# Optimization experiments

Hardware: AMD Instinct MI355X
Metric: run time of the kernel (lower is better)

The kernel has to match this reference:

```python
import jax, jax.numpy as jnp
import numpy as np

N, E, C, H, W = 5000, 80000, 32, 8, 8


def setup_inputs() -> dict:
    key = jax.random.key(0)
    k1, k2, k3, k4, k5, k6 = jax.random.split(key, 6)
    h = jax.random.normal(k1, (N, C, H, W), dtype=jnp.float32)
    e = jax.random.uniform(k2, (E,), dtype=jnp.float32)
    src = jax.random.randint(k3, (E,), 0, N, dtype=jnp.int32)
    # ensure every node receives at least one message (avoids -inf segments),
    # matching a connected graph where update_all covers all nodes
    dst = jnp.concatenate([jnp.arange(N, dtype=jnp.int32),
                           jax.random.randint(k4, (E - N,), 0, N, dtype=jnp.int32)])
    fan_in = C * 3 * 3
    bound = float(1.0 / np.sqrt(fan_in))
    conv_w = jax.random.uniform(k5, (C, C, 3, 3), minval=-bound, maxval=bound, dtype=jnp.float32)
    conv_b = jax.random.uniform(k6, (C,), minval=-bound, maxval=bound, dtype=jnp.float32)
    return {"h": h, "e": e, "conv_w": conv_w, "conv_b": conv_b, "src": src, "dst": dst}


def reference(h, e, conv_w, conv_b, src, dst):
    # message: gather source features per edge, scale by scalar edge weight
    m = e[:, None, None, None] * h[src]                      # [E, C, H, W]
    # conv2d(dim->dim, k=3, pad=1) + exact GELU, edges as batch dim
    m = jax.lax.conv_general_dilated(
        m, conv_w, window_strides=(1, 1), padding='SAME',
        dimension_numbers=('NCHW', 'OIHW', 'NCHW'))
    m = jax.nn.gelu(m + conv_b[None, :, None, None], approximate=False)
    # reduce: ragged max over each destination node's mailbox
    out = jax.ops.segment_max(m, dst, num_segments=h.shape[0])  # [N, C, H, W]
    return out
```

## Files before the change

kernel.cpp:

```cpp
#include <hip/hip_runtime.h>
#include <math.h>

#define CCH   32
#define HWPIX 64
#define CHW   2048
#define HT_STRIDE 40
#define HT_NODE   2600

typedef __attribute__((ext_vector_type(8))) short bf16x8;
typedef __attribute__((ext_vector_type(4))) float f32x4;
typedef unsigned int uint_t;
typedef unsigned short ushort_t;

__device__ __forceinline__ ushort_t f2bf(float f) {
    uint_t u = __float_as_uint(f);
    u += 0x7fffu + ((u >> 16) & 1u);
    return (ushort_t)(u >> 16);
}

__device__ __forceinline__ float fgelu(float x) {
    float x2 = x * x;
    float t = x * fmaf(0.0713548162726f, x2, 1.5957691216f);
    float ez = __expf(-t);
    return x * __builtin_amdgcn_rcpf(1.0f + ez);
}


__global__ __launch_bounds__(256) void hist_prep_kernel(
    const int* __restrict__ dst, int* cnt, int ne, int nhist,
    const float* __restrict__ w, ushort_t* __restrict__ wfrag) {
    int b = blockIdx.x;
    if (b < nhist) {
        int i = b * 256 + threadIdx.x;
        if (i < ne) atomicAdd(&cnt[dst[i]], 1);
    } else {
        for (int idx = threadIdx.x; idx < 18 * 64; idx += 256) {
            int ch = idx / (9 * 64);
            int rem = idx % (9 * 64);
            int tap = rem / 64;
            int l = rem % 64;
            int co = ch * 16 + (l & 15);
            int g = l >> 4;
            for (int j = 0; j < 8; j++) {
                int ci = g * 8 + j;
                wfrag[(size_t)idx * 8 + j] = f2bf(w[(co * CCH + ci) * 9 + tap]);
            }
        }
    }
}

__global__ __launch_bounds__(256) void scan_kernel(const int* __restrict__ cnt,
                                                   int* __restrict__ offs,
                                                   int* __restrict__ cursor,
                                                   int nn) {
    __shared__ int part[256];
    int t = threadIdx.x;
    int per = (nn + 255) >> 8;
    if (per > 32) per = 32;
    int base = t * per;
    int local[32];
    int sum = 0;
    for (int i = 0; i < per; i++) {
        int idx = base + i;
        int v = (idx < nn) ? cnt[idx] : 0;
        local[i] = sum;
        sum += v;
    }
    part[t] = sum;
    __syncthreads();
    int acc = sum;
    for (int d = 1; d < 256; d <<= 1) {
        int tv = (t >= d) ? part[t - d] : 0;
        __syncthreads();
        acc += tv;
        part[t] = acc;
        __syncthreads();
    }
    int excl = acc - sum;
    for (int i = 0; i < per; i++) {
        int idx = base + i;
        if (idx < nn) {
            int o = excl + local[i];
            offs[idx] = o;
            cursor[idx] = o;
        }
    }
    if (t == 255) offs[nn] = acc;
}

__global__ __launch_bounds__(256) void conv_scatter_kernel(
    const float* __restrict__ h, const ushort_t* __restrict__ wfrag,
    ushort_t* __restrict__ convh, int nconv,
    const int* __restrict__ dst, const int* __restrict__ src,
    const float* __restrict__ e, int* cursor, int2* __restrict__ swA, int ne) {
    __shared__ ushort_t Ht[2 * HT_NODE];
    int b = blockIdx.x;
    int t = threadIdx.x;

    if (b >= nconv) {
        int i = (b - nconv) * 256 + t;
        if (i < ne) {
            int p = atomicAdd(&cursor[dst[i]], 1);
            int2 v;
            v.x = src[i];
            v.y = __float_as_int(e[i]);
            swA[p] = v;
        }
        return;
    }

    int node0 = b * 2;
    uint_t* Hd = (uint_t*)Ht;
#pragma unroll
    for (int nd = 0; nd < 2; nd++) {
        const float* hn = h + (size_t)(node0 + nd) * CHW;
#pragma unroll
        for (int it = 0; it < 4; it++) {
            int ci2 = it * 4 + (t >> 6);
            int p = t & 63;
            float a = hn[ci2 * 128 + p];
            float bb = hn[ci2 * 128 + 64 + p];
            uint_t val = (uint_t)f2bf(a) | ((uint_t)f2bf(bb) << 16);
            Hd[nd * (HT_NODE / 2) + p * (HT_STRIDE / 2) + ci2] = val;
        }
    }
    if (t < 40) Hd[0 * (HT_NODE / 2) + 64 * (HT_STRIDE / 2) + (t % 20)] = 0;
    if (t >= 40 && t < 80) Hd[1 * (HT_NODE / 2) + 64 * (HT_STRIDE / 2) + (t - 40) % 20] = 0;
    __syncthreads();

    int l = t & 63;
    int w = __builtin_amdgcn_readfirstlane(t >> 6);
    int nd = w >> 1;
    int ch = w & 1;
    int s = l & 15, g = l >> 4;
    int n = node0 + nd;

    bf16x8 A[9];
#pragma unroll
    for (int tap = 0; tap < 9; tap++)
        A[tap] = ((const bf16x8*)wfrag)[(ch * 9 + tap) * 64 + l];

    f32x4 C[4];
#pragma unroll
    for (int i = 0; i < 4; i++) C[i] = (f32x4){0.f, 0.f, 0.f, 0.f};

    const short* HtS = (const short*)(Ht + nd * HT_NODE);
#pragma unroll
    for (int tau = 0; tau < 4; tau++) {
        int p = tau * 16 + s;
        int y = p >> 3, x = p & 7;
#pragma unroll
        for (int tap = 0; tap < 9; tap++) {
            int dy = tap / 3 - 1, dx = tap % 3 - 1;
            int yy = y + dy, xx = x + dx;
            bool valid = (yy >= 0) & (yy < 8) & (xx >= 0) & (xx < 8);
            int pp = valid ? (yy * 8 + xx) : 64;
            bf16x8 B = *(const bf16x8*)&HtS[pp * HT_STRIDE + g * 8];
            C[tau] = __builtin_amdgcn_mfma_f32_16x16x32_bf16(A[tap], B, C[tau], 0, 0, 0);
        }
    }

    ushort_t* outn = convh + (size_t)n * CHW;
#pragma unroll
    for (int tau = 0; tau < 4; tau++) {
        uint_t lo = (uint_t)f2bf(C[tau][0]) | ((uint_t)f2bf(C[tau][1]) << 16);
        uint_t hi = (uint_t)f2bf(C[tau][2]) | ((uint_t)f2bf(C[tau][3]) << 16);
        uint2 v; v.x = lo; v.y = hi;
        *(uint2*)(outn + (tau * 16 + s) * 32 + ch * 16 + g * 4) = v;
    }
}

__device__ __forceinline__ void red8(float* mn, float* mx, uint4 q, float wg) {
    uint_t u0 = q.x, u1 = q.y, u2 = q.z, u3 = q.w;
    float v;
    v = wg * __uint_as_float(u0 << 16);          mn[0] = fminf(mn[0], v); mx[0] = fmaxf(mx[0], v);
    v = wg * __uint_as_float(u0 & 0xffff0000u);  mn[1] = fminf(mn[1], v); mx[1] = fmaxf(mx[1], v);
    v = wg * __uint_as_float(u1 << 16);          mn[2] = fminf(mn[2], v); mx[2] = fmaxf(mx[2], v);
    v = wg * __uint_as_float(u1 & 0xffff0000u);  mn[3] = fminf(mn[3], v); mx[3] = fmaxf(mx[3], v);
    v = wg * __uint_as_float(u2 << 16);          mn[4] = fminf(mn[4], v); mx[4] = fmaxf(mx[4], v);
    v = wg * __uint_as_float(u2 & 0xffff0000u);  mn[5] = fminf(mn[5], v); mx[5] = fmaxf(mx[5], v);
    v = wg * __uint_as_float(u3 << 16);          mn[6] = fminf(mn[6], v); mx[6] = fmaxf(mx[6], v);
    v = wg * __uint_as_float(u3 & 0xffff0000u);  mn[7] = fminf(mn[7], v); mx[7] = fmaxf(mx[7], v);
}

__global__ __launch_bounds__(256) void gather_max_kernel(
    const ushort_t* __restrict__ convh, const float* __restrict__ bias,
    const int* __restrict__ offs, const int2* __restrict__ swA,
    float* __restrict__ out) {
    int t = threadIdx.x;
    int l = t & 63;
    int w = t >> 6;
    int b = blockIdx.x;
    int q = b & 3;
    int n = (b >> 2) * 4 + w;
    int beg = offs[n], end = offs[n + 1];
    int last = end - 1;

    const char* qbase = (const char*)convh + 1024 * q + 16 * l;

    float mn[8], mx[8];
#pragma unroll
    for (int i = 0; i < 8; i++) { mn[i] = 3.402823466e+38f; mx[i] = -3.402823466e+38f; }

    int j1 = (beg + 1 < last) ? beg + 1 : last;
    int j2 = (beg + 2 < last) ? beg + 2 : last;
    int j3 = (beg + 3 < last) ? beg + 3 : last;
    int2 d0 = swA[beg], d1 = swA[j1], d2 = swA[j2], d3 = swA[j3];
    uint4 Q0 = *(const uint4*)(qbase + (size_t)d0.x * 4096);
    uint4 Q1 = *(const uint4*)(qbase + (size_t)d1.x * 4096);
    uint4 Q2 = *(const uint4*)(qbase + (size_t)d2.x * 4096);
    uint4 Q3 = *(const uint4*)(qbase + (size_t)d3.x * 4096);
    float W0 = __int_as_float(d0.y), W1 = __int_as_float(d1.y);
    float W2 = __int_as_float(d2.y), W3 = __int_as_float(d3.y);
    int k0 = (beg + 4 < last) ? beg + 4 : last;
    int k1 = (beg + 5 < last) ? beg + 5 : last;
    int k2 = (beg + 6 < last) ? beg + 6 : last;
    int k3 = (beg + 7 < last) ? beg + 7 : last;
    int2 S0 = swA[k0], S1 = swA[k1], S2 = swA[k2], S3 = swA[k3];

    for (int j = beg; j < end; j += 4) {
        int m0 = (j + 8 < last) ? j + 8 : last;
        int m1 = (j + 9 < last) ? j + 9 : last;
        int m2 = (j + 10 < last) ? j + 10 : last;
        int m3 = (j + 11 < last) ? j + 11 : last;
        int2 N0 = swA[m0], N1 = swA[m1], N2 = swA[m2], N3 = swA[m3];
        red8(mn, mx, Q0, W0);
        Q0 = *(const uint4*)(qbase + (size_t)S0.x * 4096); W0 = __int_as_float(S0.y);
        red8(mn, mx, Q1, W1);
        Q1 = *(const uint4*)(qbase + (size_t)S1.x * 4096); W1 = __int_as_float(S1.y);
        red8(mn, mx, Q2, W2);
        Q2 = *(const uint4*)(qbase + (size_t)S2.x * 4096); W2 = __int_as_float(S2.y);
        red8(mn, mx, Q3, W3);
        Q3 = *(const uint4*)(qbase + (size_t)S3.x * 4096); W3 = __int_as_float(S3.y);
        S0 = N0; S1 = N1; S2 = N2; S3 = N3;
    }

    const float4* b4 = (const float4*)(bias + (l & 3) * 8);
    float4 bLo = b4[0], bHi = b4[1];
    float bb[8] = {bLo.x, bLo.y, bLo.z, bLo.w, bHi.x, bHi.y, bHi.z, bHi.w};
    float* op = out + (size_t)n * CHW + (size_t)(l & 3) * 512 + q * 16 + (l >> 2);
#pragma unroll
    for (int i = 0; i < 8; i++) {
        op[i * 64] = fmaxf(fgelu(mx[i] + bb[i]), fgelu(mn[i] + bb[i]));
    }
}

extern "C" void kernel_launch(void* const* d_in, const int* in_sizes, int n_in,
                              void* d_out, int out_size, void* d_ws, size_t ws_size,
                              hipStream_t stream) {
    const float* h      = (const float*)d_in[0];
    const float* e      = (const float*)d_in[1];
    const float* conv_w = (const float*)d_in[2];
    const float* conv_b = (const float*)d_in[3];
    const int*   src    = (const int*)d_in[4];
    const int*   dst    = (const int*)d_in[5];
    int nn = in_sizes[0] / CHW;
    int ne = in_sizes[1];

    ushort_t* convh = (ushort_t*)d_ws;
    ushort_t* wfrag = convh + (size_t)nn * CHW;
    int*   cnt    = (int*)(wfrag + 18 * 64 * 8);
    int*   offs   = cnt + nn;
    int*   cursor = offs + nn + 2;
    int2*  swA    = (int2*)(cursor + nn);

    int nhist = (ne + 255) / 256;
    int nconv = nn / 2;

    hipMemsetAsync(cnt, 0, (size_t)nn * sizeof(int), stream);
    hist_prep_kernel<<<nhist + 1, 256, 0, stream>>>(dst, cnt, ne, nhist,
                                                    conv_w, wfrag);
    scan_kernel<<<1, 256, 0, stream>>>(cnt, offs, cursor, nn);
    conv_scatter_kernel<<<nconv + nhist, 256, 0, stream>>>(
        h, wfrag, convh, nconv, dst, src, e, cursor, swA, ne);
    gather_max_kernel<<<nn, 256, 0, stream>>>(convh, conv_b, offs, swA,
                                              (float*)d_out);
}
```

Baseline: 153.7 us.

## Fuse scan into histogram via last-block pattern and split gather across half-waves

The histogram/weight-prep kernel now ends with an atomic completion counter, and the last block to finish performs the prefix scan, removing a separate single-block scan launch. The gather-max kernel is split into twice as many blocks, each covering half the per-node slice. Within a wave the two 32-lane halves process alternating edges and are combined with a cross-half shuffle before the GELU and store. This is meant to cut launch overhead and raise parallelism and memory-level concurrency in the gather. In exchange it adds atomics and a relaxed-load dependency in the scan, and uses half the lanes during the epilogue.

```diff
diff --git a/kernel.cpp b/kernel.cpp
--- a/kernel.cpp
+++ b/kernel.cpp
@@ -25,16 +25,17 @@
     return x * __builtin_amdgcn_rcpf(1.0f + ez);
 }
 
-
-__global__ __launch_bounds__(256) void hist_prep_kernel(
+__global__ __launch_bounds__(256) void hist_prep_scan_kernel(
     const int* __restrict__ dst, int* cnt, int ne, int nhist,
-    const float* __restrict__ w, ushort_t* __restrict__ wfrag) {
+    const float* __restrict__ w, ushort_t* __restrict__ wfrag,
+    int* __restrict__ offs, int* __restrict__ cursor, int* done, int nn) {
     int b = blockIdx.x;
+    int t = threadIdx.x;
     if (b < nhist) {
-        int i = b * 256 + threadIdx.x;
+        int i = b * 256 + t;
         if (i < ne) atomicAdd(&cnt[dst[i]], 1);
     } else {
-        for (int idx = threadIdx.x; idx < 18 * 64; idx += 256) {
+        for (int idx = t; idx < 18 * 64; idx += 256) {
             int ch = idx / (9 * 64);
             int rem = idx % (9 * 64);
             int tap = rem / 64;
@@ -47,14 +48,15 @@
             }
         }
     }
-}
-
-__global__ __launch_bounds__(256) void scan_kernel(const int* __restrict__ cnt,
-                                                   int* __restrict__ offs,
-                                                   int* __restrict__ cursor,
-                                                   int nn) {
+    __syncthreads();
+    __shared__ int s_old;
+    if (t == 0)
+        s_old = __hip_atomic_fetch_add(done, 1, __ATOMIC_ACQ_REL,
+                                       __HIP_MEMORY_SCOPE_AGENT);
+    __syncthreads();
+    if (s_old != nhist) return;
+
     __shared__ int part[256];
-    int t = threadIdx.x;
     int per = (nn + 255) >> 8;
     if (per > 32) per = 32;
     int base = t * per;
@@ -62,7 +64,10 @@
     int sum = 0;
     for (int i = 0; i < per; i++) {
         int idx = base + i;
-        int v = (idx < nn) ? cnt[idx] : 0;
+        int v = 0;
+        if (idx < nn)
+            v = __hip_atomic_load(&cnt[idx], __ATOMIC_RELAXED,
+                                  __HIP_MEMORY_SCOPE_AGENT);
         local[i] = sum;
         sum += v;
     }
@@ -191,57 +196,66 @@
     int l = t & 63;
     int w = t >> 6;
     int b = blockIdx.x;
-    int q = b & 3;
-    int n = (b >> 2) * 4 + w;
+    int q = b & 7;
+    int n = (b >> 3) * 4 + w;
     int beg = offs[n], end = offs[n + 1];
     int last = end - 1;
-
-    const char* qbase = (const char*)convh + 1024 * q + 16 * l;
+    int he = l >> 5;
+
+    const char* sbase = (const char*)convh + 512 * q + 16 * (l & 31);
 
     float mn[8], mx[8];
 #pragma unroll
     for (int i = 0; i < 8; i++) { mn[i] = 3.402823466e+38f; mx[i] = -3.402823466e+38f; }
 
-    int j1 = (beg + 1 < last) ? beg + 1 : last;
-    int j2 = (beg + 2 < last) ? beg + 2 : last;
-    int j3 = (beg + 3 < last) ? beg + 3 : last;
-    int2 d0 = swA[beg], d1 = swA[j1], d2 = swA[j2], d3 = swA[j3];
-    uint4 Q0 = *(const uint4*)(qbase + (size_t)d0.x * 4096);
-    uint4 Q1 = *(const uint4*)(qbase + (size_t)d1.x * 4096);
-    uint4 Q2 = *(const uint4*)(qbase + (size_t)d2.x * 4096);
-    uint4 Q3 = *(const uint4*)(qbase + (size_t)d3.x * 4096);
+#define IDX(j) (((j) < last) ? (j) : last)
+    int2 d0 = swA[IDX(beg + 0 + he)];
+    int2 d1 = swA[IDX(beg + 2 + he)];
+    int2 d2 = swA[IDX(beg + 4 + he)];
+    int2 d3 = swA[IDX(beg + 6 + he)];
+    uint4 Q0 = *(const uint4*)(sbase + (size_t)d0.x * 4096);
+    uint4 Q1 = *(const uint4*)(sbase + (size_t)d1.x * 4096);
+    uint4 Q2 = *(const uint4*)(sbase + (size_t)d2.x * 4096);
+    uint4 Q3 = *(const uint4*)(sbase + (size_t)d3.x * 4096);
     float W0 = __int_as_float(d0.y), W1 = __int_as_float(d1.y);
     float W2 = __int_as_float(d2.y), W3 = __int_as_float(d3.y);
-    int k0 = (beg + 4 < last) ? beg + 4 : last;
-    int k1 = (beg + 5 < last) ? beg + 5 : last;
-    int k2 = (beg + 6 < last) ? beg + 6 : last;
-    int k3 = (beg + 7 < last) ? beg + 7 : last;
-    int2 S0 = swA[k0], S1 = swA[k1], S2 = swA[k2], S3 = swA[k3];
-
-    for (int j = beg; j < end; j += 4) {
-        int m0 = (j + 8 < last) ? j + 8 : last;
-        int m1 = (j + 9 < last) ? j + 9 : last;
-        int m2 = (j + 10 < last) ? j + 10 : last;
-        int m3 = (j + 11 < last) ? j + 11 : last;
-        int2 N0 = swA[m0], N1 = swA[m1], N2 = swA[m2], N3 = swA[m3];
+    int2 S0 = swA[IDX(beg + 8 + he)];
+    int2 S1 = swA[IDX(beg + 10 + he)];
+    int2 S2 = swA[IDX(beg + 12 + he)];
+    int2 S3 = swA[IDX(beg + 14 + he)];
+
+    for (int j = beg; j < end; j += 8) {
+        int2 N0 = swA[IDX(j + 16 + he)];
+        int2 N1 = swA[IDX(j + 18 + he)];
+        int2 N2 = swA[IDX(j + 20 + he)];
+        int2 N3 = swA[IDX(j + 22 + he)];
         red8(mn, mx, Q0, W0);
-        Q0 = *(const uint4*)(qbase + (size_t)S0.x * 4096); W0 = __int_as_float(S0.y);
+        Q0 = *(const uint4*)(sbase + (size_t)S0.x * 4096); W0 = __int_as_float(S0.y);
         red8(mn, mx, Q1, W1);
-        Q1 = *(const uint4*)(qbase + (size_t)S1.x * 4096); W1 = __int_as_float(S1.y);
+        Q1 = *(const uint4*)(sbase + (size_t)S1.x * 4096); W1 = __int_as_float(S1.y);
         red8(mn, mx, Q2, W2);
-        Q2 = *(const uint4*)(qbase + (size_t)S2.x * 4096); W2 = __int_as_float(S2.y);
+        Q2 = *(const uint4*)(sbase + (size_t)S2.x * 4096); W2 = __int_as_float(S2.y);
         red8(mn, mx, Q3, W3);
-        Q3 = *(const uint4*)(qbase + (size_t)S3.x * 4096); W3 = __int_as_float(S3.y);
+        Q3 = *(const uint4*)(sbase + (size_t)S3.x * 4096); W3 = __int_as_float(S3.y);
         S0 = N0; S1 = N1; S2 = N2; S3 = N3;
     }
-
-    const float4* b4 = (const float4*)(bias + (l & 3) * 8);
-    float4 bLo = b4[0], bHi = b4[1];
-    float bb[8] = {bLo.x, bLo.y, bLo.z, bLo.w, bHi.x, bHi.y, bHi.z, bHi.w};
-    float* op = out + (size_t)n * CHW + (size_t)(l & 3) * 512 + q * 16 + (l >> 2);
+#undef IDX
+
 #pragma unroll
     for (int i = 0; i < 8; i++) {
-        op[i * 64] = fmaxf(fgelu(mx[i] + bb[i]), fgelu(mn[i] + bb[i]));
+        mn[i] = fminf(mn[i], __shfl_xor(mn[i], 32));
+        mx[i] = fmaxf(mx[i], __shfl_xor(mx[i], 32));
+    }
+
+    if (l < 32) {
+        const float4* b4 = (const float4*)(bias + (l & 3) * 8);
+        float4 bLo = b4[0], bHi = b4[1];
+        float bb[8] = {bLo.x, bLo.y, bLo.z, bLo.w, bHi.x, bHi.y, bHi.z, bHi.w};
+        float* op = out + (size_t)n * CHW + (size_t)(l & 3) * 512 + q * 8 + (l >> 2);
+#pragma unroll
+        for (int i = 0; i < 8; i++) {
+            op[i * 64] = fmaxf(fgelu(mx[i] + bb[i]), fgelu(mn[i] + bb[i]));
+        }
     }
 }
 
@@ -260,19 +274,19 @@
     ushort_t* convh = (ushort_t*)d_ws;
     ushort_t* wfrag = convh + (size_t)nn * CHW;
     int*   cnt    = (int*)(wfrag + 18 * 64 * 8);
-    int*   offs   = cnt + nn;
+    int*   done   = cnt + nn;
+    int*   offs   = done + 1;
     int*   cursor = offs + nn + 2;
     int2*  swA    = (int2*)(cursor + nn);
 
     int nhist = (ne + 255) / 256;
     int nconv = nn / 2;
 
-    hipMemsetAsync(cnt, 0, (size_t)nn * sizeof(int), stream);
-    hist_prep_kernel<<<nhist + 1, 256, 0, stream>>>(dst, cnt, ne, nhist,
-                                                    conv_w, wfrag);
-    scan_kernel<<<1, 256, 0, stream>>>(cnt, offs, cursor, nn);
+    hipMemsetAsync(cnt, 0, (size_t)(nn + 1) * sizeof(int), stream);
+    hist_prep_scan_kernel<<<nhist + 1, 256, 0, stream>>>(
+        dst, cnt, ne, nhist, conv_w, wfrag, offs, cursor, done, nn);
     conv_scatter_kernel<<<nconv + nhist, 256, 0, stream>>>(
         h, wfrag, convh, nconv, dst, src, e, cursor, swA, ne);
-    gather_max_kernel<<<nn, 256, 0, stream>>>(convh, conv_b, offs, swA,
-                                              (float*)d_out);
-}
+    gather_max_kernel<<<(nn / 4) * 8, 256, 0, stream>>>(convh, conv_b, offs, swA,
+                                                        (float*)d_out);
+}
```

Result: slower. 167.5 us (+9.0%).
